# Performance work log

Hardware: AMD Instinct MI355X
Metric: run time of the kernel (lower is better)

Reference implementation:

```python
import jax, jax.numpy as jnp
import numpy as np

B, C, H, W = 8, 512, 64, 64


def conv3x3(x, w, b):
    # x: [B,C,H,W], w: [O,I,3,3], b: [O]; stride 1, padding 1 (SAME)
    y = jax.lax.conv_general_dilated(
        x, w, window_strides=(1, 1), padding='SAME',
        dimension_numbers=('NCHW', 'OIHW', 'NCHW'))
    return y + b[None, :, None, None]


def setup_inputs() -> dict:
    key = jax.random.key(0)
    ks = jax.random.split(key, 8)
    wscale = 1.0 / np.sqrt(C * 9)  # keep attention logits in a sane range
    x = jax.random.normal(ks[0], (B, C, H, W), dtype=jnp.float32)
    wq = jax.random.normal(ks[1], (C, C, 3, 3), dtype=jnp.float32) * wscale
    bq = jax.random.normal(ks[2], (C,), dtype=jnp.float32) * 0.01
    wk = jax.random.normal(ks[3], (C, C, 3, 3), dtype=jnp.float32) * wscale
    bk = jax.random.normal(ks[4], (C,), dtype=jnp.float32) * 0.01
    wv = jax.random.normal(ks[5], (C, C, 3, 3), dtype=jnp.float32) * wscale
    bv = jax.random.normal(ks[6], (C,), dtype=jnp.float32) * 0.01
    gamma = jax.random.normal(ks[7], (1,), dtype=jnp.float32)
    return {'x': x, 'wq': wq, 'bq': bq, 'wk': wk, 'bk': bk,
            'wv': wv, 'bv': bv, 'gamma': gamma}


def reference(x, wq, bq, wk, bk, wv, bv, gamma):
    b, c, h, w = x.shape
    n = h * w
    q = conv3x3(x, wq, bq).reshape(b, c, n)   # [B,C,N]
    k = conv3x3(x, wk, bk).reshape(b, c, n)   # [B,C,N]
    v = conv3x3(x, wv, bv).reshape(b, c, n)   # [B,C,N]
    # channel-wise attention: [B,C,N] x [B,N,C] -> [B,C,C]
    attn = jnp.einsum('bcn,bdn->bcd', q, k)
    attn = jax.nn.softmax(attn, axis=-1)
    out = jnp.einsum('bcd,bdn->bcn', attn, v).reshape(b, c, h, w)
    return gamma * out + x
```

## Files before the change

kernel.cpp:

```cpp
#include <hip/hip_runtime.h>
#include <stdint.h>

typedef __attribute__((ext_vector_type(8))) short bf16x8;
typedef __attribute__((ext_vector_type(4))) float f32x4;
typedef __attribute__((ext_vector_type(2))) long i64x2;
typedef __attribute__((ext_vector_type(8))) unsigned short u16x8;
typedef __attribute__((ext_vector_type(4))) unsigned short u16x4;

#define DI static __device__ __forceinline__

constexpr int CB = 8;
constexpr int BCH = 4;
constexpr int CC = 512;
constexpr int CN = 4096;
constexpr int K1 = CC * 9;
constexpr int MR = 3 * CC;
constexpr int KSPL = 4;
constexpr size_t XSPLIT = (size_t)BCH * 66 * 66 * 512;

DI unsigned short f2bf(float f) {
  union { float f; uint32_t u; } v; v.f = f;
  uint32_t r = (v.u + 0x7FFFu + ((v.u >> 16) & 1u)) >> 16;
  return (unsigned short)r;
}
DI float bf2f(unsigned short h) {
  union { uint32_t u; float f; } v; v.u = ((uint32_t)h) << 16;
  return v.f;
}
DI unsigned char f2e4m3(float x) {
  union { float f; uint32_t u; } v; v.f = x;
  uint32_t sgn = (v.u >> 24) & 0x80u;
  float a = fabsf(x);
  if (a < 0.015625f) {
    int qi = (int)rintf(a * 512.f);
    return (unsigned char)(sgn | (uint32_t)qi);
  }
  int e = (int)((v.u >> 23) & 0xff) - 127;
  uint32_t m3 = (v.u >> 20) & 7u;
  uint32_t rest = v.u & 0xFFFFFu;
  if (rest > 0x80000u || (rest == 0x80000u && (m3 & 1u))) {
    if (++m3 == 8u) { m3 = 0; ++e; }
  }
  if (e > 8 || (e == 8 && m3 == 7u)) return (unsigned char)(sgn | 0x7Eu);
  return (unsigned char)(sgn | ((uint32_t)(e + 7) << 3) | m3);
}
DI int perm64(int k) { return (k & 7) + (((k >> 5) & 1) << 3) + (((k >> 3) & 3) << 4); }

DI void g2lds16(const void* g, void* l) {
  __builtin_amdgcn_global_load_lds((const __attribute__((address_space(1))) void*)g,
                                   (__attribute__((address_space(3))) void*)l, 16, 0, 0);
}
#define SBAR()  __builtin_amdgcn_s_barrier()
#define SCHED() __builtin_amdgcn_sched_barrier(0)

__global__ __launch_bounds__(256) void prep_xpad(const float* __restrict__ x,
                                                 unsigned short* __restrict__ Xhi,
                                                 unsigned char* __restrict__ X8) {
  int tid = threadIdx.x;
  int w = tid & 63;
  int ccl = tid >> 6;
  int blk = blockIdx.x;
  int h = blk & 63;
  int ccg = (blk >> 6) & 15;
  int b = blk >> 10;
  int c0 = (ccg * 4 + ccl) * 8;
  const float* xp = x + ((size_t)b * CC) * CN + h * 64 + w;
  u16x8 hi;
  unsigned long long lo8 = 0, hi8 = 0;
#pragma unroll
  for (int j = 0; j < 8; ++j) {
    float v = xp[(size_t)(c0 + j) * CN];
    unsigned short h16 = f2bf(v);
    float vhi = bf2f(h16);
    hi[j] = f2bf(vhi * 128.f);
    lo8 |= (unsigned long long)f2e4m3((v - vhi) * 256.f) << (8 * j);
    hi8 |= (unsigned long long)f2e4m3(vhi) << (8 * j);
  }
  size_t pix = (((size_t)b * 66 + (h + 1)) * 66 + (w + 1)) * 512;
  *(u16x8*)&Xhi[pix + c0] = hi;
  size_t p8 = pix + (size_t)(c0 & ~63) + perm64(c0 & 63);
  *(unsigned long long*)&X8[p8] = lo8;
  *(unsigned long long*)&X8[XSPLIT + p8] = hi8;
}

__global__ __launch_bounds__(256) void prep_abig(
    const float* __restrict__ wq, const float* __restrict__ wk,
    const float* __restrict__ wv, const float* __restrict__ bq,
    const float* __restrict__ bk, const float* __restrict__ bv,
    unsigned short* __restrict__ Ahi, unsigned char* __restrict__ A8,
    float* __restrict__ bias) {
  unsigned id = blockIdx.x * 256 + threadIdx.x;
  int m = id / K1;
  int r = id - m * K1;
  int t = r >> 9;
  int c = r & 511;
  int ky = t / 3;
  int kx = t - ky * 3;
  size_t ip = (size_t)m * 9216 + (size_t)(r & ~63) + perm64(r & 63);
  if (m < 1024) {
    const float* wp = (m < 512) ? wq : wk;
    int mm = (m < 512) ? m : m - 512;
    float wval = wp[(((size_t)mm * 512 + c) * 3 + ky) * 3 + kx];
    float whi = bf2f(f2bf(wval));
    Ahi[id] = f2bf(whi * 128.f);
    A8[ip] = f2e4m3(whi * 64.f);
    A8[ip + 4608] = f2e4m3((wval - whi) * 16384.f);
  } else {
    float wval = wv[(((size_t)(m - 1024) * 512 + c) * 3 + ky) * 3 + kx];
    Ahi[id] = f2bf(wval * 128.f);
    A8[ip] = 0;
    A8[ip + 4608] = 0;
  }
  if (id < 1536) {
    int mm = (int)id;
    bias[mm] = (mm < 512) ? bq[mm] : (mm < 1024) ? bk[mm - 512] : bv[mm - 1024];
  }
}

__global__ __launch_bounds__(512, 2) void conv_k(
    const unsigned short* __restrict__ Ahi,
    const unsigned char* __restrict__ A8,
    const unsigned short* __restrict__ Xhi,
    const unsigned char* __restrict__ X8,
    const float* __restrict__ bias,
    unsigned short* __restrict__ Qhi, unsigned short* __restrict__ Qlo,
    unsigned short* __restrict__ Khi, unsigned short* __restrict__ Klo,
    unsigned short* __restrict__ Vt)
{
  __shared__ __align__(16) unsigned char smem[4 * 32768];
  const int tid = threadIdx.x;
  const int lane = tid & 63;
  const int wid = tid >> 6;
  const int wr = wid >> 2;
  const int wc = wid & 3;

  int orig = blockIdx.x;
  int xcd, nbl, mb;
  if (orig < 256) { xcd = orig & 7; int j = orig >> 3; nbl = j >> 2; mb = j & 3; }
  else { int o = orig - 256; xcd = o & 7; int j = o >> 3; nbl = j >> 1; mb = 4 + (j & 1); }
  const int nb = xcd * 8 + nbl;
  const int m0 = mb * 256;
  const int n0 = nb * 256;
  const int bidx = n0 >> 12;
  const int nl0 = n0 & (CN - 1);
  const int h0 = nl0 >> 6;

  const int srow = tid >> 2;
  const int scu = tid & 3;
  const int scuS = scu ^ ((srow >> 1) & 3);
  const size_t pixOfs = (((size_t)(bidx * 66 + h0 + (srow >> 6))) * 66 + (srow & 63)) * 512;
  const unsigned short* gAh0 = Ahi + (size_t)(m0 + srow) * K1 + scuS * 8;
  const unsigned short* gAh1 = gAh0 + (size_t)128 * K1;
  const unsigned short* gBh0 = Xhi + pixOfs + scuS * 8;
  const unsigned short* gBh1 = gBh0 + (size_t)2 * 66 * 512;
  const unsigned char* gA80 = A8 + (size_t)(m0 + srow) * 9216 + scuS * 16;
  const unsigned char* gA81 = gA80 + (size_t)128 * 9216;
  const unsigned char* gB80 = X8 + pixOfs + scuS * 16;
  const unsigned char* gB81 = gB80 + (size_t)2 * 66 * 512;
  const int wofs = wid * 1024;

  int c0S = 0, kxS = 0, tapS = 0;
  size_t tapOfs = 0;
  auto stage1 = [&](int slot) {
    int aOfs = tapS * 512 + c0S;
    size_t bOfs = tapOfs + (size_t)c0S;
    unsigned char* lA = smem + slot * 32768 + wofs;
    unsigned char* lB = smem + slot * 32768 + 16384 + wofs;
    g2lds16(gAh0 + aOfs, lA);
    g2lds16(gAh1 + aOfs, lA + 8192);
    g2lds16(gBh0 + bOfs, lB);
    g2lds16(gBh1 + bOfs, lB + 8192);
    c0S += 32;
    if (c0S == 512) {
      c0S = 0; ++tapS;
      if (kxS == 2) { kxS = 0; tapOfs += (size_t)64 * 512; }
      else { ++kxS; tapOfs += 512; }
    }
  };
  int c8 = 0, kx8 = 0, tap8 = 0, s8 = 0;
  size_t tapOfs8 = 0;
  auto stage2 = [&](int slot) {
    int aOfs = s8 * 4608 + tap8 * 512 + c8;
    size_t bOfs = (size_t)s8 * XSPLIT + tapOfs8 + (size_t)c8;
    unsigned char* lA = smem + slot * 32768 + wofs;
    unsigned char* lB = smem + slot * 32768 + 16384 + wofs;
    g2lds16(gA80 + aOfs, lA);
    g2lds16(gA81 + aOfs, lA + 8192);
    g2lds16(gB80 + bOfs, lB);
    g2lds16(gB81 + bOfs, lB + 8192);
    c8 += 64;
    if (c8 == 512) {
      c8 = 0; ++tap8;
      if (tap8 == 9) { tap8 = 0; kx8 = 0; tapOfs8 = 0; ++s8; }
      else if (kx8 == 2) { kx8 = 0; tapOfs8 += (size_t)64 * 512; }
      else { ++kx8; tapOfs8 += 512; }
    }
  };

  f32x4 acc[8][4];
  const f32x4 fz = {0.f, 0.f, 0.f, 0.f};
#pragma unroll
  for (int i = 0; i < 8; ++i)
#pragma unroll
    for (int j = 0; j < 4; ++j) acc[i][j] = fz;

  const int rA = wr * 128 + (lane & 15);
  const int rB = wc * 64 + (lane & 15);
  const int kq = (lane >> 4) * 16;
  const int kqA = kq ^ (((rA >> 1) & 3) << 4);
  const int kqB = kq ^ (((rB >> 1) & 3) << 4);

  int slotC, slotS, t2;

  stage1(0);
  stage1(1);
  asm volatile("s_waitcnt vmcnt(4)" ::: "memory");
  SCHED(); SBAR(); SCHED();
  {
    bf16x8 afA[4], bfA[4], afB[4], bfB[4], af1[4];
#pragma unroll
    for (int mf = 0; mf < 4; ++mf)
      afA[mf] = *(const bf16x8*)(smem + (rA + mf * 16) * 64 + kqA);
#pragma unroll
    for (int nf = 0; nf < 4; ++nf)
      bfA[nf] = *(const bf16x8*)(smem + 16384 + (rB + nf * 16) * 64 + kqB);
    slotC = 0; slotS = 2; t2 = 2;

#define CONV_BF(CURA, CURB, NXTA, NXTB)                                       \
  {                                                                           \
    if (t2 < 144) {                                                           \
      stage1(slotS); slotS = (slotS + 1) & 3;                                 \
      asm volatile("s_waitcnt vmcnt(4)" ::: "memory");                        \
    } else {                                                                  \
      asm volatile("s_waitcnt vmcnt(0)" ::: "memory");                        \
    }                                                                         \
    SCHED(); SBAR(); SCHED();                                                 \
    const unsigned char* lA = smem + slotC * 32768;                           \
    const int slotN = (slotC + 1) & 3;                                        \
    const unsigned char* lAn = smem + slotN * 32768;                          \
    _Pragma("unroll")                                                         \
    for (int mf = 0; mf < 4; ++mf)                                            \
      af1[mf] = *(const bf16x8*)(lA + (rA + 64 + mf * 16) * 64 + kqA);        \
    __builtin_amdgcn_s_setprio(1);                                            \
    _Pragma("unroll")                                                         \
    for (int mf = 0; mf < 4; ++mf) {                                          \
      _Pragma("unroll")                                                       \
      for (int nf = 0; nf < 4; ++nf)                                          \
        acc[mf][nf] = __builtin_amdgcn_mfma_f32_16x16x32_bf16(                \
            CURA[mf], CURB[nf], acc[mf][nf], 0, 0, 0);                        \
    }                                                                         \
    __builtin_amdgcn_s_setprio(0);                                            \
    _Pragma("unroll")                                                         \
    for (int mf = 0; mf < 4; ++mf)                                            \
      NXTA[mf] = *(const bf16x8*)(lAn + (rA + mf * 16) * 64 + kqA);           \
    _Pragma("unroll")                                                         \
    for (int nf = 0; nf < 4; ++nf)                                            \
      NXTB[nf] = *(const bf16x8*)(lAn + 16384 + (rB + nf * 16) * 64 + kqB);   \
    __builtin_amdgcn_s_setprio(1);                                            \
    _Pragma("unroll")                                                         \
    for (int mf = 0; mf < 4; ++mf) {                                          \
      _Pragma("unroll")                                                       \
      for (int nf = 0; nf < 4; ++nf)                                          \
        acc[mf + 4][nf] = __builtin_amdgcn_mfma_f32_16x16x32_bf16(            \
            af1[mf], CURB[nf], acc[mf + 4][nf], 0, 0, 0);                     \
    }                                                                         \
    __builtin_amdgcn_s_setprio(0);                                            \
    slotC = slotN;                                                            \
    ++t2;                                                                     \
  }

    for (int t = 0; t < 144; t += 2) {
      CONV_BF(afA, bfA, afB, bfB)
      CONV_BF(afB, bfB, afA, bfA)
    }
#undef CONV_BF
  }

  if (m0 < 1024) {
    stage2(0);
    stage2(1);
    asm volatile("s_waitcnt vmcnt(4)" ::: "memory");
    SCHED(); SBAR(); SCHED();
    i64x2 a8A[4], b8A[4], a8B[4], b8B[4], a18[4];
#pragma unroll
    for (int mf = 0; mf < 4; ++mf)
      a8A[mf] = *(const i64x2*)(smem + (rA + mf * 16) * 64 + kqA);
#pragma unroll
    for (int nf = 0; nf < 4; ++nf)
      b8A[nf] = *(const i64x2*)(smem + 16384 + (rB + nf * 16) * 64 + kqB);
    slotC = 0; slotS = 2; t2 = 2;

#define CONV_F8(CURA, CURB, NXTA, NXTB)                                       \
  {                                                                           \
    if (t2 < 144) {                                                           \
      stage2(slotS); slotS = (slotS + 1) & 3;                                 \
      asm volatile("s_waitcnt vmcnt(4)" ::: "memory");                        \
    } else {                                                                  \
      asm volatile("s_waitcnt vmcnt(0)" ::: "memory");                        \
    }                                                                         \
    SCHED(); SBAR(); SCHED();                                                 \
    const unsigned char* lA = smem + slotC * 32768;                           \
    const int slotN = (slotC + 1) & 3;                                        \
    const unsigned char* lAn = smem + slotN * 32768;                          \
    _Pragma("unroll")                                                         \
    for (int mf = 0; mf < 4; ++mf)                                            \
      a18[mf] = *(const i64x2*)(lA + (rA + 64 + mf * 16) * 64 + kqA);         \
    __builtin_amdgcn_s_setprio(1);                                            \
    _Pragma("unroll")                                                         \
    for (int mf = 0; mf < 4; ++mf) {                                          \
      _Pragma("unroll")                                                       \
      for (int nf = 0; nf < 4; ++nf) {                                        \
        acc[mf][nf] = __builtin_amdgcn_mfma_f32_16x16x32_fp8_fp8(             \
            CURA[mf][0], CURB[nf][0], acc[mf][nf], 0, 0, 0);                  \
        acc[mf][nf] = __builtin_amdgcn_mfma_f32_16x16x32_fp8_fp8(             \
            CURA[mf][1], CURB[nf][1], acc[mf][nf], 0, 0, 0);                  \
      }                                                                       \
    }                                                                         \
    __builtin_amdgcn_s_setprio(0);                                            \
    _Pragma("unroll")                                                         \
    for (int mf = 0; mf < 4; ++mf)                                            \
      NXTA[mf] = *(const i64x2*)(lAn + (rA + mf * 16) * 64 + kqA);            \
    _Pragma("unroll")                                                         \
    for (int nf = 0; nf < 4; ++nf)                                            \
      NXTB[nf] = *(const i64x2*)(lAn + 16384 + (rB + nf * 16) * 64 + kqB);    \
    __builtin_amdgcn_s_setprio(1);                                            \
    _Pragma("unroll")                                                         \
    for (int mf = 0; mf < 4; ++mf) {                                          \
      _Pragma("unroll")                                                       \
      for (int nf = 0; nf < 4; ++nf) {                                        \
        acc[mf + 4][nf] = __builtin_amdgcn_mfma_f32_16x16x32_fp8_fp8(         \
            a18[mf][0], CURB[nf][0], acc[mf + 4][nf], 0, 0, 0);               \
        acc[mf + 4][nf] = __builtin_amdgcn_mfma_f32_16x16x32_fp8_fp8(         \
            a18[mf][1], CURB[nf][1], acc[mf + 4][nf], 0, 0, 0);               \
      }                                                                       \
    }                                                                         \
    __builtin_amdgcn_s_setprio(0);                                            \
    slotC = slotN;                                                            \
    ++t2;                                                                     \
  }

    for (int t = 0; t < 144; t += 2) {
      CONV_F8(a8A, b8A, a8B, b8B)
      CONV_F8(a8B, b8B, a8A, b8A)
    }
#undef CONV_F8
  }

  constexpr float SC = 1.f / 16384.f;
#pragma unroll
  for (int mf = 0; mf < 8; ++mf) {
#pragma unroll
    for (int nf = 0; nf < 4; ++nf) {
      f32x4 a = acc[mf][nf];
      int mrow = m0 + wr * 128 + mf * 16 + ((lane >> 4) << 2);
      int ncol = nl0 + wc * 64 + nf * 16 + (lane & 15);
      if (m0 < 512) {
#pragma unroll
        for (int j = 0; j < 4; ++j) {
          float v = a[j] * SC + bias[mrow + j];
          unsigned short h16 = f2bf(v);
          size_t o = ((size_t)bidx * CC + (mrow + j)) * CN + ncol;
          Qhi[o] = h16;
          Qlo[o] = f2bf(v - bf2f(h16));
        }
      } else if (m0 < 1024) {
#pragma unroll
        for (int j = 0; j < 4; ++j) {
          float v = a[j] * SC + bias[mrow + j];
          unsigned short h16 = f2bf(v);
          size_t o = ((size_t)bidx * CC + (mrow + j - 512)) * CN + ncol;
          Khi[o] = h16;
          Klo[o] = f2bf(v - bf2f(h16));
        }
      } else {
        u16x4 vs;
#pragma unroll
        for (int j = 0; j < 4; ++j) vs[j] = f2bf(a[j] * SC + bias[mrow + j]);
        *(u16x4*)&Vt[((size_t)bidx * CN + ncol) * CC + (mrow - 1024)] = vs;
      }
    }
  }
}

DI int sofs(int row, int kb) { return row * 128 + (kb ^ ((row & 7) << 4)); }

template<int MODE>
__global__ __launch_bounds__(256) void gemm_k(
    const unsigned short* __restrict__ Qhi, const unsigned short* __restrict__ Qlo,
    const unsigned short* __restrict__ Khi, const unsigned short* __restrict__ Klo,
    const unsigned short* __restrict__ Vt,
    float* __restrict__ attn,
    const unsigned short* __restrict__ P,
    const float* __restrict__ xin,
    const float* __restrict__ gamma,
    float* __restrict__ out)
{
  __shared__ __align__(16) unsigned char sA[16384];
  __shared__ __align__(16) unsigned char sB[16384];
  const int tid = threadIdx.x;
  const int lane = tid & 63;
  const int wav = tid >> 6;
  const int wr = wav >> 1, wc = wav & 1;

  int m0, n0, bidx, Kbeg = 0, Kend, ks = 0;
  if constexpr (MODE == 1) {
    int tile = blockIdx.x & 15;
    ks = blockIdx.x >> 4;
    m0 = (tile & 3) * 128;
    n0 = (tile >> 2) * 128;
    bidx = blockIdx.z;
    Kbeg = ks * (3 * CN / KSPL);
    Kend = Kbeg + (3 * CN / KSPL);
  } else {
    m0 = (blockIdx.x & 3) * 128;
    n0 = (blockIdx.x >> 2) * 128;
    bidx = blockIdx.z;
    Kend = CC;
  }

  auto stage = [&](int k0) {
#pragma unroll
    for (int q = 0; q < 4; ++q) {
      int ci = q * 256 + tid;
      int row = ci >> 3;
      int ke = ((ci & 7) ^ (row & 7)) * 8;
      const unsigned short* ap;
      const unsigned short* bp;
      if constexpr (MODE == 1) {
        int ph = k0 >> 12;
        int kin = k0 & (CN - 1);
        const unsigned short* Aq = (ph == 2) ? Qlo : Qhi;
        const unsigned short* Bk = (ph == 1) ? Klo : Khi;
        ap = Aq + ((size_t)bidx * CC + (m0 + row)) * CN + (kin + ke);
        bp = Bk + ((size_t)bidx * CC + (n0 + row)) * CN + (kin + ke);
      } else {
        ap = P + ((size_t)bidx * CC + (m0 + row)) * CC + (k0 + ke);
        bp = Vt + ((size_t)bidx * CN + (n0 + row)) * CC + (k0 + ke);
      }
      int wbase = (q * 256 + wav * 64) * 16;
      g2lds16(ap, sA + wbase);
      g2lds16(bp, sB + wbase);
    }
  };

  f32x4 acc[4][4];
  const f32x4 fz = {0.f, 0.f, 0.f, 0.f};
#pragma unroll
  for (int i = 0; i < 4; ++i)
#pragma unroll
    for (int j = 0; j < 4; ++j) acc[i][j] = fz;

  for (int k0 = Kbeg; k0 < Kend; k0 += 64) {
    stage(k0);
    __syncthreads();
#pragma unroll
    for (int kkp = 0; kkp < 2; ++kkp) {
      bf16x8 af[4], bfv[4];
#pragma unroll
      for (int mf = 0; mf < 4; ++mf)
        af[mf] = *(const bf16x8*)&sA[sofs(wr * 64 + mf * 16 + (lane & 15),
                                          kkp * 64 + (lane >> 4) * 16)];
#pragma unroll
      for (int nf = 0; nf < 4; ++nf)
        bfv[nf] = *(const bf16x8*)&sB[sofs(wc * 64 + nf * 16 + (lane & 15),
                                           kkp * 64 + (lane >> 4) * 16)];
#pragma unroll
      for (int mf = 0; mf < 4; ++mf)
#pragma unroll
        for (int nf = 0; nf < 4; ++nf)
          acc[mf][nf] = __builtin_amdgcn_mfma_f32_16x16x32_bf16(
              af[mf], bfv[nf], acc[mf][nf], 0, 0, 0);
    }
    __syncthreads();
  }

  float g = 0.f;
  if constexpr (MODE == 2) g = gamma[0];
#pragma unroll
  for (int mf = 0; mf < 4; ++mf) {
#pragma unroll
    for (int nf = 0; nf < 4; ++nf) {
      f32x4 a = acc[mf][nf];
      int mrow = m0 + wr * 64 + mf * 16 + ((lane >> 4) << 2);
      int ncol = n0 + wc * 64 + nf * 16 + (lane & 15);
      if constexpr (MODE == 1) {
        size_t pbase = (size_t)ks * ((size_t)BCH * CC * CC);
#pragma unroll
        for (int j = 0; j < 4; ++j)
          attn[pbase + ((size_t)bidx * CC + (mrow + j)) * CC + ncol] = a[j];
      } else {
#pragma unroll
        for (int j = 0; j < 4; ++j) {
          size_t o = ((size_t)bidx * CC + (mrow + j)) * CN + ncol;
          out[o] = g * a[j] + xin[o];
        }
      }
    }
  }
}

__global__ __launch_bounds__(256) void softmax_k(const float* __restrict__ attn,
                                                 unsigned short* __restrict__ P) {
  int row = blockIdx.x * 4 + (threadIdx.x >> 6);
  int lane = threadIdx.x & 63;
  constexpr size_t PS = (size_t)BCH * CC * CC;
  const float* rp = attn + (size_t)row * 512 + lane * 8;
  f32x4 a = {0.f, 0.f, 0.f, 0.f};
  f32x4 b = {0.f, 0.f, 0.f, 0.f};
#pragma unroll
  for (int ksp = 0; ksp < KSPL; ++ksp) {
    a += *(const f32x4*)(rp + (size_t)ksp * PS);
    b += *(const f32x4*)(rp + (size_t)ksp * PS + 4);
  }
  float mx = fmaxf(fmaxf(fmaxf(a[0], a[1]), fmaxf(a[2], a[3])),
                   fmaxf(fmaxf(b[0], b[1]), fmaxf(b[2], b[3])));
#pragma unroll
  for (int s = 32; s > 0; s >>= 1) mx = fmaxf(mx, __shfl_xor(mx, s, 64));
  float e[8];
  float sum = 0.f;
#pragma unroll
  for (int j = 0; j < 4; ++j) { e[j] = __expf(a[j] - mx); sum += e[j]; }
#pragma unroll
  for (int j = 0; j < 4; ++j) { e[4 + j] = __expf(b[j] - mx); sum += e[4 + j]; }
#pragma unroll
  for (int s = 32; s > 0; s >>= 1) sum += __shfl_xor(sum, s, 64);
  float inv = 1.0f / sum;
  u16x8 o;
#pragma unroll
  for (int j = 0; j < 8; ++j) o[j] = f2bf(e[j] * inv);
  *(u16x8*)&P[(size_t)row * 512 + lane * 8] = o;
}

__global__ __launch_bounds__(256) void fill_sentinel(float* __restrict__ out, int n) {
  int i = blockIdx.x * 256 + threadIdx.x;
  if (i < n) out[i] = 1.0e4f;
}

extern "C" void kernel_launch(void* const* d_in, const int* in_sizes, int n_in,
                              void* d_out, int out_size, void* d_ws, size_t ws_size,
                              hipStream_t stream) {
  (void)in_sizes; (void)n_in;
  const float* x  = (const float*)d_in[0];
  const float* wq = (const float*)d_in[1];
  const float* bq = (const float*)d_in[2];
  const float* wk = (const float*)d_in[3];
  const float* bk = (const float*)d_in[4];
  const float* wv = (const float*)d_in[5];
  const float* bv = (const float*)d_in[6];
  const float* gm = (const float*)d_in[7];
  float* out = (float*)d_out;

  uint8_t* wsp = (uint8_t*)d_ws;
  auto take = [&](size_t bytes) {
    uint8_t* p = wsp;
    wsp += (bytes + 255) & ~(size_t)255;
    return p;
  };
  unsigned short* Xhi = (unsigned short*)take(XSPLIT * 2);
  unsigned char*  X8  = (unsigned char*)take(2 * XSPLIT);
  unsigned short* Ahi = (unsigned short*)take((size_t)MR * K1 * 2);
  unsigned char*  A8  = (unsigned char*)take((size_t)MR * 2 * K1);
  float* bias         = (float*)take((size_t)MR * 4);
  unsigned short* Khi = (unsigned short*)take((size_t)BCH * CC * CN * 2);
  unsigned short* Klo = (unsigned short*)take((size_t)BCH * CC * CN * 2);
  unsigned short* Vt  = (unsigned short*)take((size_t)BCH * CN * CC * 2);
  float* attn         = (float*)Xhi;
  unsigned short* P   = (unsigned short*)((uint8_t*)Xhi +
                          (size_t)KSPL * BCH * CC * CC * 4 + 256);

  size_t needed = (size_t)(wsp - (uint8_t*)d_ws);
  if (ws_size < needed) {
    fill_sentinel<<<(out_size + 255) / 256, 256, 0, stream>>>(out, out_size);
    return;
  }

  for (int ch = 0; ch < CB / BCH; ++ch) {
    const float* xch = x + (size_t)ch * BCH * CC * CN;
    float* outch = out + (size_t)ch * BCH * CC * CN;
    unsigned short* Qhi = (unsigned short*)outch;
    unsigned short* Qlo = Qhi + (size_t)BCH * CC * CN;

    hipMemsetAsync(Xhi, 0, XSPLIT * 2 + 2 * XSPLIT, stream);
    prep_xpad<<<BCH * 16 * 64, 256, 0, stream>>>(xch, Xhi, X8);
    if (ch == 0)
      prep_abig<<<(MR * K1) / 256, 256, 0, stream>>>(wq, wk, wv, bq, bk, bv,
                                                     Ahi, A8, bias);
    conv_k<<<dim3(6 * BCH * 16), 512, 0, stream>>>(Ahi, A8, Xhi, X8, bias,
                                                   Qhi, Qlo, Khi, Klo, Vt);
    gemm_k<1><<<dim3(16 * KSPL, 1, BCH), 256, 0, stream>>>(Qhi, Qlo, Khi, Klo, Vt,
                                                           attn, P, xch, gm, outch);
    softmax_k<<<BCH * 128, 256, 0, stream>>>(attn, P);
    gemm_k<2><<<dim3(128, 1, BCH), 256, 0, stream>>>(Qhi, Qlo, Khi, Klo, Vt,
                                                     attn, P, xch, gm, outch);
  }
}
```

Baseline: 1.112 ms.

## Split V-projection conv into 128-row tiles to balance block work

The V-output blocks of the conv kernel (which only run the bf16 pass, not the extra fp8 correction pass) are re-tiled from 256 output rows to 128 rows. This doubles their block count, so the grid grows from 384 to 512 blocks. A dedicated staging lambda and MFMA loop handle the half-height A tile. The aim is to even out per-block work between the Q/K blocks (two passes) and the V blocks (one pass) and fill more CUs. The cost is lower arithmetic intensity for the V tiles, since B is reloaded for half the rows.

```diff
diff --git a/kernel.cpp b/kernel.cpp
--- a/kernel.cpp
+++ b/kernel.cpp
@@ -135,11 +135,18 @@
   const int wc = wid & 3;
 
   int orig = blockIdx.x;
-  int xcd, nbl, mb;
-  if (orig < 256) { xcd = orig & 7; int j = orig >> 3; nbl = j >> 2; mb = j & 3; }
-  else { int o = orig - 256; xcd = o & 7; int j = o >> 3; nbl = j >> 1; mb = 4 + (j & 1); }
+  int xcd, nbl, m0;
+  if (orig < 256) {
+    xcd = orig & 7; int j = orig >> 3;
+    nbl = j >> 2;
+    m0 = (j & 3) * 256;
+  } else {
+    int o = orig - 256;
+    xcd = o & 7; int j = o >> 3;
+    nbl = j >> 2;
+    m0 = 1024 + (j & 3) * 128;
+  }
   const int nb = xcd * 8 + nbl;
-  const int m0 = mb * 256;
   const int n0 = nb * 256;
   const int bidx = n0 >> 12;
   const int nl0 = n0 & (CN - 1);
@@ -168,6 +175,21 @@
     unsigned char* lB = smem + slot * 32768 + 16384 + wofs;
     g2lds16(gAh0 + aOfs, lA);
     g2lds16(gAh1 + aOfs, lA + 8192);
+    g2lds16(gBh0 + bOfs, lB);
+    g2lds16(gBh1 + bOfs, lB + 8192);
+    c0S += 32;
+    if (c0S == 512) {
+      c0S = 0; ++tapS;
+      if (kxS == 2) { kxS = 0; tapOfs += (size_t)64 * 512; }
+      else { ++kxS; tapOfs += 512; }
+    }
+  };
+  auto stage1v = [&](int slot) {
+    int aOfs = tapS * 512 + c0S;
+    size_t bOfs = tapOfs + (size_t)c0S;
+    unsigned char* lA = smem + slot * 32768 + wofs;
+    unsigned char* lB = smem + slot * 32768 + 16384 + wofs;
+    g2lds16(gAh0 + aOfs, lA);
     g2lds16(gBh0 + bOfs, lB);
     g2lds16(gBh1 + bOfs, lB + 8192);
     c0S += 32;
@@ -204,27 +226,28 @@
 #pragma unroll
     for (int j = 0; j < 4; ++j) acc[i][j] = fz;
 
-  const int rA = wr * 128 + (lane & 15);
-  const int rB = wc * 64 + (lane & 15);
   const int kq = (lane >> 4) * 16;
-  const int kqA = kq ^ (((rA >> 1) & 3) << 4);
-  const int kqB = kq ^ (((rB >> 1) & 3) << 4);
-
   int slotC, slotS, t2;
 
-  stage1(0);
-  stage1(1);
-  asm volatile("s_waitcnt vmcnt(4)" ::: "memory");
-  SCHED(); SBAR(); SCHED();
-  {
-    bf16x8 afA[4], bfA[4], afB[4], bfB[4], af1[4];
-#pragma unroll
-    for (int mf = 0; mf < 4; ++mf)
-      afA[mf] = *(const bf16x8*)(smem + (rA + mf * 16) * 64 + kqA);
-#pragma unroll
-    for (int nf = 0; nf < 4; ++nf)
-      bfA[nf] = *(const bf16x8*)(smem + 16384 + (rB + nf * 16) * 64 + kqB);
-    slotC = 0; slotS = 2; t2 = 2;
+  if (m0 < 1024) {
+    const int rA = wr * 128 + (lane & 15);
+    const int rB = wc * 64 + (lane & 15);
+    const int kqA = kq ^ (((rA >> 1) & 3) << 4);
+    const int kqB = kq ^ (((rB >> 1) & 3) << 4);
+
+    stage1(0);
+    stage1(1);
+    asm volatile("s_waitcnt vmcnt(4)" ::: "memory");
+    SCHED(); SBAR(); SCHED();
+    {
+      bf16x8 afA[4], bfA[4], afB[4], bfB[4], af1[4];
+#pragma unroll
+      for (int mf = 0; mf < 4; ++mf)
+        afA[mf] = *(const bf16x8*)(smem + (rA + mf * 16) * 64 + kqA);
+#pragma unroll
+      for (int nf = 0; nf < 4; ++nf)
+        bfA[nf] = *(const bf16x8*)(smem + 16384 + (rB + nf * 16) * 64 + kqB);
+      slotC = 0; slotS = 2; t2 = 2;
 
 #define CONV_BF(CURA, CURB, NXTA, NXTB)                                       \
   {                                                                           \
@@ -269,26 +292,26 @@
     ++t2;                                                                     \
   }
 
-    for (int t = 0; t < 144; t += 2) {
-      CONV_BF(afA, bfA, afB, bfB)
-      CONV_BF(afB, bfB, afA, bfA)
-    }
+      for (int t = 0; t < 144; t += 2) {
+        CONV_BF(afA, bfA, afB, bfB)
+        CONV_BF(afB, bfB, afA, bfA)
+      }
 #undef CONV_BF
-  }
-
-  if (m0 < 1024) {
-    stage2(0);
-    stage2(1);
-    asm volatile("s_waitcnt vmcnt(4)" ::: "memory");
-    SCHED(); SBAR(); SCHED();
-    i64x2 a8A[4], b8A[4], a8B[4], b8B[4], a18[4];
-#pragma unroll
-    for (int mf = 0; mf < 4; ++mf)
-      a8A[mf] = *(const i64x2*)(smem + (rA + mf * 16) * 64 + kqA);
-#pragma unroll
-    for (int nf = 0; nf < 4; ++nf)
-      b8A[nf] = *(const i64x2*)(smem + 16384 + (rB + nf * 16) * 64 + kqB);
-    slotC = 0; slotS = 2; t2 = 2;
+    }
+
+    {
+      stage2(0);
+      stage2(1);
+      asm volatile("s_waitcnt vmcnt(4)" ::: "memory");
+      SCHED(); SBAR(); SCHED();
+      i64x2 a8A[4], b8A[4], a8B[4], b8B[4], a18[4];
+#pragma unroll
+      for (int mf = 0; mf < 4; ++mf)
+        a8A[mf] = *(const i64x2*)(smem + (rA + mf * 16) * 64 + kqA);
+#pragma unroll
+      for (int nf = 0; nf < 4; ++nf)
+        b8A[nf] = *(const i64x2*)(smem + 16384 + (rB + nf * 16) * 64 + kqB);
+      slotC = 0; slotS = 2; t2 = 2;
 
 #define CONV_F8(CURA, CURB, NXTA, NXTB)                                       \
   {                                                                           \
@@ -339,40 +362,106 @@
     ++t2;                                                                     \
   }
 
+      for (int t = 0; t < 144; t += 2) {
+        CONV_F8(a8A, b8A, a8B, b8B)
+        CONV_F8(a8B, b8B, a8A, b8A)
+      }
+#undef CONV_F8
+    }
+  } else {
+    const int rAv = wr * 64 + (lane & 15);
+    const int rB = wc * 64 + (lane & 15);
+    const int kqA = kq ^ (((rAv >> 1) & 3) << 4);
+    const int kqB = kq ^ (((rB >> 1) & 3) << 4);
+
+    stage1v(0);
+    stage1v(1);
+    asm volatile("s_waitcnt vmcnt(3)" ::: "memory");
+    SCHED(); SBAR(); SCHED();
+    bf16x8 afA[4], bfA[4], afB[4], bfB[4];
+#pragma unroll
+    for (int mf = 0; mf < 4; ++mf)
+      afA[mf] = *(const bf16x8*)(smem + (rAv + mf * 16) * 64 + kqA);
+#pragma unroll
+    for (int nf = 0; nf < 4; ++nf)
+      bfA[nf] = *(const bf16x8*)(smem + 16384 + (rB + nf * 16) * 64 + kqB);
+    slotC = 0; slotS = 2; t2 = 2;
+
+#define CONV_LV(CURA, CURB, NXTA, NXTB)                                       \
+  {                                                                           \
+    if (t2 < 144) {                                                           \
+      stage1v(slotS); slotS = (slotS + 1) & 3;                                \
+      asm volatile("s_waitcnt vmcnt(3)" ::: "memory");                        \
+    } else {                                                                  \
+      asm volatile("s_waitcnt vmcnt(0)" ::: "memory");                        \
+    }                                                                         \
+    SCHED(); SBAR(); SCHED();                                                 \
+    const int slotN = (slotC + 1) & 3;                                        \
+    const unsigned char* lAn = smem + slotN * 32768;                          \
+    _Pragma("unroll")                                                         \
+    for (int mf = 0; mf < 4; ++mf)                                            \
+      NXTA[mf] = *(const bf16x8*)(lAn + (rAv + mf * 16) * 64 + kqA);          \
+    _Pragma("unroll")                                                         \
+    for (int nf = 0; nf < 4; ++nf)                                            \
+      NXTB[nf] = *(const bf16x8*)(lAn + 16384 + (rB + nf * 16) * 64 + kqB);   \
+    __builtin_amdgcn_s_setprio(1);                                            \
+    _Pragma("unroll")                                                         \
+    for (int mf = 0; mf < 4; ++mf) {                                          \
+      _Pragma("unroll")                                                       \
+      for (int nf = 0; nf < 4; ++nf)                                          \
+        acc[mf][nf] = __builtin_amdgcn_mfma_f32_16x16x32_bf16(                \
+            CURA[mf], CURB[nf], acc[mf][nf], 0, 0, 0);                        \
+    }                                                                         \
+    __builtin_amdgcn_s_setprio(0);                                            \
+    slotC = slotN;                                                            \
+    ++t2;                                                                     \
+  }
+
     for (int t = 0; t < 144; t += 2) {
-      CONV_F8(a8A, b8A, a8B, b8B)
-      CONV_F8(a8B, b8B, a8A, b8A)
-    }
-#undef CONV_F8
+      CONV_LV(afA, bfA, afB, bfB)
+      CONV_LV(afB, bfB, afA, bfA)
+    }
+#undef CONV_LV
   }
 
   constexpr float SC = 1.f / 16384.f;
-#pragma unroll
-  for (int mf = 0; mf < 8; ++mf) {
-#pragma unroll
-    for (int nf = 0; nf < 4; ++nf) {
-      f32x4 a = acc[mf][nf];
-      int mrow = m0 + wr * 128 + mf * 16 + ((lane >> 4) << 2);
-      int ncol = nl0 + wc * 64 + nf * 16 + (lane & 15);
-      if (m0 < 512) {
-#pragma unroll
-        for (int j = 0; j < 4; ++j) {
-          float v = a[j] * SC + bias[mrow + j];
-          unsigned short h16 = f2bf(v);
-          size_t o = ((size_t)bidx * CC + (mrow + j)) * CN + ncol;
-          Qhi[o] = h16;
-          Qlo[o] = f2bf(v - bf2f(h16));
+  if (m0 < 1024) {
+#pragma unroll
+    for (int mf = 0; mf < 8; ++mf) {
+#pragma unroll
+      for (int nf = 0; nf < 4; ++nf) {
+        f32x4 a = acc[mf][nf];
+        int mrow = m0 + wr * 128 + mf * 16 + ((lane >> 4) << 2);
+        int ncol = nl0 + wc * 64 + nf * 16 + (lane & 15);
+        if (m0 < 512) {
+#pragma unroll
+          for (int j = 0; j < 4; ++j) {
+            float v = a[j] * SC + bias[mrow + j];
+            unsigned short h16 = f2bf(v);
+            size_t o = ((size_t)bidx * CC + (mrow + j)) * CN + ncol;
+            Qhi[o] = h16;
+            Qlo[o] = f2bf(v - bf2f(h16));
+          }
+        } else {
+#pragma unroll
+          for (int j = 0; j < 4; ++j) {
+            float v = a[j] * SC + bias[mrow + j];
+            unsigned short h16 = f2bf(v);
+            size_t o = ((size_t)bidx * CC + (mrow + j - 512)) * CN + ncol;
+            Khi[o] = h16;
+            Klo[o] = f2bf(v - bf2f(h16));
+          }
         }
-      } else if (m0 < 1024) {
-#pragma unroll
-        for (int j = 0; j < 4; ++j) {
-          float v = a[j] * SC + bias[mrow + j];
-          unsigned short h16 = f2bf(v);
-          size_t o = ((size_t)bidx * CC + (mrow + j - 512)) * CN + ncol;
-          Khi[o] = h16;
-          Klo[o] = f2bf(v - bf2f(h16));
-        }
-      } else {
+      }
+    }
+  } else {
+#pragma unroll
+    for (int mf = 0; mf < 4; ++mf) {
+#pragma unroll
+      for (int nf = 0; nf < 4; ++nf) {
+        f32x4 a = acc[mf][nf];
+        int mrow = m0 + wr * 64 + mf * 16 + ((lane >> 4) << 2);
+        int ncol = nl0 + wc * 64 + nf * 16 + (lane & 15);
         u16x4 vs;
 #pragma unroll
         for (int j = 0; j < 4; ++j) vs[j] = f2bf(a[j] * SC + bias[mrow + j]);
@@ -585,8 +674,8 @@
     if (ch == 0)
       prep_abig<<<(MR * K1) / 256, 256, 0, stream>>>(wq, wk, wv, bq, bk, bv,
                                                      Ahi, A8, bias);
-    conv_k<<<dim3(6 * BCH * 16), 512, 0, stream>>>(Ahi, A8, Xhi, X8, bias,
-                                                   Qhi, Qlo, Khi, Klo, Vt);
+    conv_k<<<dim3(512), 512, 0, stream>>>(Ahi, A8, Xhi, X8, bias,
+                                          Qhi, Qlo, Khi, Klo, Vt);
     gemm_k<1><<<dim3(16 * KSPL, 1, BCH), 256, 0, stream>>>(Qhi, Qlo, Khi, Klo, Vt,
                                                            attn, P, xch, gm, outch);
     softmax_k<<<BCH * 128, 256, 0, stream>>>(attn, P);
```

New measurement: 1.054 ms. -5.2%, faster.
